# Optimization experiments

Measured on AMD Instinct MI355X. Metric: run time of the kernel, lower is better.

Reference implementation:

```python
import jax, jax.numpy as jnp
import numpy as np

N, E, DIN, DH, DE, DOUT, G = 100000, 1600000, 64, 128, 16, 1, 256

def setup_inputs() -> dict:
    key = jax.random.key(0)
    ks = jax.random.split(key, 16)
    p = lambda k, s: (jax.random.normal(k, s, dtype=jnp.float32) * 0.05)
    return {
        "x": jax.random.normal(ks[0], (N, DIN), dtype=jnp.float32),
        "edge_index": jax.random.randint(ks[1], (2, E), 0, N, dtype=jnp.int64),
        "edge_attr": jax.random.normal(ks[2], (E, DE), dtype=jnp.float32),
        "batch": jnp.sort(jax.random.randint(ks[3], (N,), 0, G, dtype=jnp.int64)),
        # GINEConv 1: edge lin (edge_dim -> input_dim) + mlp1 (DIN->DH->DH)
        "ew1": p(ks[4], (DIN, DE)), "eb1": p(ks[5], (DIN,)),
        "w1a": p(ks[6], (DH, DIN)), "b1a": p(ks[7], (DH,)),
        "w1b": p(ks[8], (DH, DH)), "b1b": p(ks[9], (DH,)),
        # GINEConv 2: edge lin (edge_dim -> hidden_dim) + mlp2 (DH->DH->DH)
        "ew2": p(ks[10], (DH, DE)), "eb2": p(ks[11], (DH,)),
        "w2a": p(ks[12], (DH, DH)), "b2a": p(ks[13], (DH,)),
        "w2b": p(ks[14], (DH, DH)), "b2b": p(ks[15], (DH,)),
        "wf": p(jax.random.fold_in(key, 99), (DOUT, DH)),
        "bf": jnp.zeros((DOUT,), dtype=jnp.float32),
    }

def _gine(x, src, dst, edge_attr, ew, eb, wa, ba, wb, bb):
    # message = relu(x[src] + Lin(edge_attr)); sum-aggregate at dst; eps=0
    msg = jax.nn.relu(x[src] + edge_attr @ ew.T + eb)          # [E, D]
    aggr = jax.ops.segment_sum(msg, dst, num_segments=x.shape[0])
    h = x + aggr                                               # (1+eps)*x + aggr, eps=0
    h = jax.nn.relu(h @ wa.T + ba)
    return h @ wb.T + bb

def reference(x, edge_index, edge_attr, batch, ew1, eb1, w1a, b1a, w1b, b1b,
              ew2, eb2, w2a, b2a, w2b, b2b, wf, bf):
    src, dst = edge_index[0], edge_index[1]
    h = _gine(x, src, dst, edge_attr, ew1, eb1, w1a, b1a, w1b, b1b)
    h = jax.nn.relu(h)  # dropout is identity in eval mode
    h = _gine(h, src, dst, edge_attr, ew2, eb2, w2a, b2a, w2b, b2b)
    h = jax.nn.relu(h)
    # global mean pool over graphs
    sums = jax.ops.segment_sum(h, batch, num_segments=G)       # [G, DH]
    cnts = jax.ops.segment_sum(jnp.ones((h.shape[0],), h.dtype), batch, num_segments=G)
    pooled = sums / jnp.maximum(cnts, 1.0)[:, None]
    return pooled @ wf.T + bf                                  # [G, DOUT]
```

## Files before the change

kernel.cpp:

```cpp
#include <hip/hip_runtime.h>

#define DINc 64
#define DHc  128
#define DEc  16
#define Gc   256
#define Rrep 64
#define SCB  1024

typedef unsigned short u16;
typedef unsigned int   u32;
typedef __attribute__((ext_vector_type(8))) short bf8;
typedef __attribute__((ext_vector_type(4))) short bf4;
typedef __attribute__((ext_vector_type(4))) float f4;
typedef __attribute__((ext_vector_type(4))) unsigned int u32x4;
typedef _Float16 h2t __attribute__((ext_vector_type(2)));

__device__ __forceinline__ u16 f2b(float f) {
  u32 u = __builtin_bit_cast(u32, f);
  u32 r = u + 0x7FFFu + ((u >> 16) & 1u);
  return (u16)(r >> 16);
}
__device__ __forceinline__ float b2f(u16 h) {
  u32 u = ((u32)h) << 16;
  return __builtin_bit_cast(float, u);
}
__device__ __forceinline__ float blo(u32 v) { return __builtin_bit_cast(float, v << 16); }
__device__ __forceinline__ float bhi(u32 v) { return __builtin_bit_cast(float, v & 0xFFFF0000u); }
__device__ __forceinline__ u32 pkbf(float a, float b) {
  return ((u32)f2b(b) << 16) | (u32)f2b(a);
}
__device__ __forceinline__ u32 pkh(float a, float b) {
  u16 ua = __builtin_bit_cast(u16, (_Float16)a);
  u16 ub = __builtin_bit_cast(u16, (_Float16)b);
  return ((u32)ub << 16) | ua;
}
__device__ __forceinline__ float fd2(u32 a, u32 b, float c) {
  return __builtin_amdgcn_fdot2(__builtin_bit_cast(h2t, a),
                                __builtin_bit_cast(h2t, b), c, false);
}

__global__ __launch_bounds__(256) void k_prep(
    const float* __restrict__ w1a, const float* __restrict__ w1b,
    const float* __restrict__ w2a, const float* __restrict__ w2b,
    u16* __restrict__ wts,
    const int* __restrict__ dstA, const int nE, int* __restrict__ deg) {
  const int b = blockIdx.x;
  if (b < 28) {
    const int i = b * 256 + threadIdx.x;
    const float* src; int off;
    if      (i < 1024) { src = w1a; off = i; }
    else if (i < 3072) { src = w1b; off = i - 1024; }
    else if (i < 5120) { src = w2a; off = i - 3072; }
    else if (i < 7168) { src = w2b; off = i - 5120; }
    else return;
    float4 f0 = *(const float4*)(src + (size_t)off * 8);
    float4 f1 = *(const float4*)(src + (size_t)off * 8 + 4);
    bf8 v;
    v[0]=(short)f2b(f0.x); v[1]=(short)f2b(f0.y); v[2]=(short)f2b(f0.z); v[3]=(short)f2b(f0.w);
    v[4]=(short)f2b(f1.x); v[5]=(short)f2b(f1.y); v[6]=(short)f2b(f1.z); v[7]=(short)f2b(f1.w);
    *(bf8*)(wts + (size_t)i * 8) = v;
  } else {
    const int nb = gridDim.x - 28;
    for (int i = (b - 28) * 256 + threadIdx.x; i < nE; i += nb * 256)
      atomicAdd(&deg[dstA[i]], 1);
  }
}

__global__ __launch_bounds__(256) void k_scan_blk(const int* __restrict__ deg,
                                                  int* __restrict__ bsum, const int nN) {
  const int b = blockIdx.x, t = threadIdx.x;
  const int i0 = b * SCB + t * 4;
  int s = 0;
  #pragma unroll
  for (int q = 0; q < 4; ++q) { const int i = i0 + q; if (i < nN) s += deg[i]; }
  #pragma unroll
  for (int off = 32; off > 0; off >>= 1) s += __shfl_down(s, off);
  __shared__ int ws[4];
  if ((t & 63) == 0) ws[t >> 6] = s;
  __syncthreads();
  if (t == 0) bsum[b] = ws[0] + ws[1] + ws[2] + ws[3];
}

__global__ __launch_bounds__(256) void k_scan_fin(const int* __restrict__ deg,
                                                  const int* __restrict__ bsum,
                                                  int* __restrict__ rowptr,
                                                  const int nN, const int nB) {
  const int b = blockIdx.x, t = threadIdx.x;
  int p = 0;
  for (int i = t; i < b; i += 256) p += bsum[i];
  #pragma unroll
  for (int off = 32; off > 0; off >>= 1) p += __shfl_down(p, off);
  __shared__ int ws[4];
  __shared__ int sc[256];
  if ((t & 63) == 0) ws[t >> 6] = p;
  const int i0 = b * SCB + t * 4;
  int vals[4]; int s = 0;
  #pragma unroll
  for (int q = 0; q < 4; ++q) { const int i = i0 + q; vals[q] = (i < nN) ? deg[i] : 0; s += vals[q]; }
  sc[t] = s;
  __syncthreads();
  const int boff = ws[0] + ws[1] + ws[2] + ws[3];
  for (int off = 1; off < 256; off <<= 1) {
    int u = (t >= off) ? sc[t - off] : 0;
    __syncthreads();
    sc[t] += u;
    __syncthreads();
  }
  int run = boff + sc[t] - s;
  #pragma unroll
  for (int q = 0; q < 4; ++q) { const int i = i0 + q; if (i < nN) rowptr[i] = run; run += vals[q]; }
  if (b == nB - 1 && t == 255) rowptr[nN] = run;
}

__global__ __launch_bounds__(256) void k_fill(const int* __restrict__ dstA,
                                              const int* __restrict__ srcA,
                                              const float* __restrict__ ea, const int nE,
                                              const int* __restrict__ rowptr,
                                              int* __restrict__ cursor,
                                              int* __restrict__ srcC,
                                              int* __restrict__ dstC,
                                              u16* __restrict__ ea16) {
  for (int i = blockIdx.x * 256 + threadIdx.x; i < nE; i += gridDim.x * 256) {
    const int d = dstA[i];
    const int pos = rowptr[d] + atomicAdd(&cursor[d], 1);
    srcC[pos] = srcA[i];
    dstC[pos] = d;
    const float4* ep = (const float4*)(ea + (size_t)i * 16);
    float4 a0 = ep[0], a1 = ep[1], a2 = ep[2], a3 = ep[3];
    u32x4 w0, w1;
    w0[0] = pkh(a0.x, a0.y); w0[1] = pkh(a0.z, a0.w);
    w0[2] = pkh(a1.x, a1.y); w0[3] = pkh(a1.z, a1.w);
    w1[0] = pkh(a2.x, a2.y); w1[1] = pkh(a2.z, a2.w);
    w1[2] = pkh(a3.x, a3.y); w1[3] = pkh(a3.z, a3.w);
    *(u32x4*)(ea16 + (size_t)pos * 16)     = w0;
    *(u32x4*)(ea16 + (size_t)pos * 16 + 8) = w1;
  }
}

__device__ __forceinline__ int span_lb(const int* __restrict__ rp, int nN, int target) {
  int lo = 0, hi = nN;
  while (lo < hi) { int m = (lo + hi) >> 1; if (rp[m] < target) lo = m + 1; else hi = m; }
  return lo;
}

#define STORE_N(NODE) do { \
  if (PL == 2) *(u32*)(agg + (size_t)(NODE) * 128 + lane * 2) = pkbf(acc0, acc1); \
  else         agg[(size_t)(NODE) * 64 + lane] = f2b(acc0); \
} while (0)
#define STORE_Z(NODE) do { \
  if (PL == 2) *(u32*)(agg + (size_t)(NODE) * 128 + lane * 2) = 0u; \
  else         agg[(size_t)(NODE) * 64 + lane] = 0; \
} while (0)
#define BCHK(EIDX) do { \
  if ((bmask >> (EIDX)) & 1ull) { \
    const int nd = __builtin_amdgcn_readlane(dl, (EIDX)); \
    if (cur >= n0) STORE_N(cur); \
    for (int m = cur + 1; m < nd; ++m) STORE_Z(m); \
    acc0 = 0.f; acc1 = 0.f; cur = nd; \
  } \
} while (0)
#define ACC_EDGE(EIDX, Q) do { \
  u32x4 r0 = *(const u32x4*)&E[(EIDX)][0]; \
  u32x4 r1 = *(const u32x4*)&E[(EIDX)][4]; \
  if (PL == 1) { \
    float v = ebr[0]; \
    v = fd2(r0[0], wpk[0], v); v = fd2(r0[1], wpk[1], v); \
    v = fd2(r0[2], wpk[2], v); v = fd2(r0[3], wpk[3], v); \
    v = fd2(r1[0], wpk[4], v); v = fd2(r1[1], wpk[5], v); \
    v = fd2(r1[2], wpk[6], v); v = fd2(r1[3], wpk[7], v); \
    const float xval = XF ? xs[Q] : blo(xv[Q]); \
    acc0 += fmaxf(xval + v, 0.f); \
  } else { \
    float v0 = ebr[0], v1 = ebr[1]; \
    v0 = fd2(r0[0], wpk[0], v0); v1 = fd2(r0[0], wpk[8],  v1); \
    v0 = fd2(r0[1], wpk[1], v0); v1 = fd2(r0[1], wpk[9],  v1); \
    v0 = fd2(r0[2], wpk[2], v0); v1 = fd2(r0[2], wpk[10], v1); \
    v0 = fd2(r0[3], wpk[3], v0); v1 = fd2(r0[3], wpk[11], v1); \
    v0 = fd2(r1[0], wpk[4], v0); v1 = fd2(r1[0], wpk[12], v1); \
    v0 = fd2(r1[1], wpk[5], v0); v1 = fd2(r1[1], wpk[13], v1); \
    v0 = fd2(r1[2], wpk[6], v0); v1 = fd2(r1[2], wpk[14], v1); \
    v0 = fd2(r1[3], wpk[7], v0); v1 = fd2(r1[3], wpk[15], v1); \
    acc0 += fmaxf(blo(xv[Q]) + v0, 0.f); \
    acc1 += fmaxf(bhi(xv[Q]) + v1, 0.f); \
  } \
} while (0)

template<int D, bool XF>
__global__ __launch_bounds__(256) void gather4(
    const float* __restrict__ xf, const u16* __restrict__ xb,
    const int* __restrict__ srcC, const int* __restrict__ dstC,
    const u16* __restrict__ ea16,
    const float* __restrict__ ewg, const float* __restrict__ ebg,
    const int* __restrict__ rowptr, u16* __restrict__ agg,
    const int nN, const int nE)
{
  constexpr int PL = D / 64;
  __shared__ u32 eas[4][64][8];
  const int lane = threadIdx.x & 63, wv = threadIdx.x >> 6;
  u32 (*E)[8] = eas[wv];

  u32 wpk[8 * PL]; float ebr[PL];
  #pragma unroll
  for (int p = 0; p < PL; ++p) {
    const int d = lane * PL + p;
    ebr[p] = ebg[d];
    #pragma unroll
    for (int j = 0; j < 8; ++j)
      wpk[p * 8 + j] = pkh(ewg[d * 16 + 2 * j], ewg[d * 16 + 2 * j + 1]);
  }

  const int wgid = blockIdx.x * 4 + wv;
  const int nw   = gridDim.x * 4;
  const int t0 = (int)((long long)nE * wgid / nw);
  const int t1 = (int)((long long)nE * (wgid + 1) / nw);
  const int n0 = span_lb(rowptr, nN, t0);
  const int n1 = (wgid == nw - 1) ? nN : span_lb(rowptr, nN, t1);
  if (n0 >= n1) return;
  const int e0 = rowptr[n0], e1 = rowptr[n1];

  float acc0 = 0.f, acc1 = 0.f;
  int cur = n0 - 1;

  for (int chunk = e0; chunk < e1; chunk += 64) {
    const int cnt = min(64, e1 - chunk);
    int sid = (lane < cnt) ? srcC[chunk + lane] : 0;
    int dl  = (lane < cnt) ? dstC[chunk + lane] : -1;
    const int pd = __shfl_up(dl, 1);
    const bool bnd = (lane < cnt) && (dl != ((lane == 0) ? cur : pd));
    const unsigned long long bmask = __ballot(bnd);

    if (lane < cnt) {
      u32x4 a = *(const u32x4*)(ea16 + (size_t)(chunk + lane) * 16);
      u32x4 b = *(const u32x4*)(ea16 + (size_t)(chunk + lane) * 16 + 8);
      *(u32x4*)&E[lane][0] = a;
      *(u32x4*)&E[lane][4] = b;
    }

    if (cnt == 64) {
      #pragma unroll 1
      for (int i = 0; i < 64; i += 8) {
        u32 xv[8]; float xs[8];
        #pragma unroll
        for (int q = 0; q < 8; ++q) {
          const int s = __builtin_amdgcn_readlane(sid, i + q);
          if (XF) xs[q] = xf[(size_t)s * D + lane];
          else    xv[q] = *(const u32*)(xb + (size_t)s * D + lane * 2);
        }
        const u32 gm = (u32)(bmask >> i) & 0xFFu;
        if (gm == 0) {
          #pragma unroll
          for (int q = 0; q < 8; ++q) ACC_EDGE(i + q, q);
        } else {
          #pragma unroll
          for (int q = 0; q < 8; ++q) { BCHK(i + q); ACC_EDGE(i + q, q); }
        }
      }
    } else {
      for (int i = 0; i < cnt; i += 8) {
        const int g = min(8, cnt - i);
        u32 xv[8]; float xs[8];
        #pragma unroll
        for (int q = 0; q < 8; ++q) {
          if (q < g) {
            const int s = __builtin_amdgcn_readlane(sid, i + q);
            if (XF) xs[q] = xf[(size_t)s * D + lane];
            else    xv[q] = *(const u32*)(xb + (size_t)s * D + lane * 2);
          }
        }
        #pragma unroll
        for (int q = 0; q < 8; ++q) {
          if (q < g) { BCHK(i + q); ACC_EDGE(i + q, q); }
        }
      }
    }
  }
  if (cur >= n0) STORE_N(cur);
  for (int m = cur + 1; m < n1; ++m) STORE_Z(m);
}

template<int IN, bool XF>
__global__ __launch_bounds__(256) void k_l1(
    const float* __restrict__ xf, const u16* __restrict__ xbm,
    const u16* __restrict__ agb,
    const u16* __restrict__ waB, const float* __restrict__ ba,
    u16* __restrict__ tout, const int nN)
{
  __shared__ u16 wa_s[DHc * IN];
  __shared__ float ba_s[DHc];
  const int tid = threadIdx.x;
  constexpr int INC = IN / 8;
  for (int c = tid; c < DHc * INC; c += 256) {
    const int row = c / INC, kc = (c % INC) * 8;
    bf8 v = *(const bf8*)(waB + (size_t)row * IN + kc);
    *(bf8*)(wa_s + ((row * IN + kc) ^ ((row & 7) << 3))) = v;
  }
  if (tid < DHc) ba_s[tid] = ba[tid];
  __syncthreads();
  const int lane = tid & 63, wv = tid >> 6;
  const int lr = lane & 15, l4 = lane >> 4;
  const int nT = (nN + 15) >> 4;
  for (int tile = blockIdx.x * 4 + wv; tile < nT; tile += gridDim.x * 4) {
    const int node = tile * 16 + lr;
    const int n = min(node, nN - 1);
    bf8 bfr[IN / 32];
    #pragma unroll
    for (int ks = 0; ks < IN / 32; ++ks) {
      const int k0 = ks * 32 + l4 * 8;
      bf8 av = *(const bf8*)(agb + (size_t)n * IN + k0);
      bf8 v;
      if (XF) {
        float4 x0 = *(const float4*)(xf + (size_t)n * IN + k0);
        float4 x1 = *(const float4*)(xf + (size_t)n * IN + k0 + 4);
        v[0] = (short)f2b(x0.x + b2f((u16)av[0]));
        v[1] = (short)f2b(x0.y + b2f((u16)av[1]));
        v[2] = (short)f2b(x0.z + b2f((u16)av[2]));
        v[3] = (short)f2b(x0.w + b2f((u16)av[3]));
        v[4] = (short)f2b(x1.x + b2f((u16)av[4]));
        v[5] = (short)f2b(x1.y + b2f((u16)av[5]));
        v[6] = (short)f2b(x1.z + b2f((u16)av[6]));
        v[7] = (short)f2b(x1.w + b2f((u16)av[7]));
      } else {
        bf8 xv = *(const bf8*)(xbm + (size_t)n * IN + k0);
        #pragma unroll
        for (int j = 0; j < 8; ++j)
          v[j] = (short)f2b(b2f((u16)xv[j]) + b2f((u16)av[j]));
      }
      bfr[ks] = v;
    }
    const bool valid = node < nN;
    #pragma unroll
    for (int jt = 0; jt < 8; ++jt) {
      f4 c = {0.f, 0.f, 0.f, 0.f};
      #pragma unroll
      for (int ks = 0; ks < IN / 32; ++ks) {
        bf8 a = *(const bf8*)(wa_s + (((jt * 16 + lr) * IN + ks * 32 + l4 * 8) ^ ((lr & 7) << 3)));
        c = __builtin_amdgcn_mfma_f32_16x16x32_bf16(a, bfr[ks], c, 0, 0, 0);
      }
      if (valid) {
        float4 bav = *(const float4*)(ba_s + jt * 16 + l4 * 4);
        bf4 tv;
        tv[0] = (short)f2b(fmaxf(c[0] + bav.x, 0.f));
        tv[1] = (short)f2b(fmaxf(c[1] + bav.y, 0.f));
        tv[2] = (short)f2b(fmaxf(c[2] + bav.z, 0.f));
        tv[3] = (short)f2b(fmaxf(c[3] + bav.w, 0.f));
        *(bf4*)(tout + (size_t)node * DHc + jt * 16 + l4 * 4) = tv;
      }
    }
  }
}

template<bool FINAL>
__global__ __launch_bounds__(256) void k_l2(
    const u16* __restrict__ tin, const u16* __restrict__ wbB,
    const float* __restrict__ bb, u16* __restrict__ hout,
    const int* __restrict__ batch, float* __restrict__ sums, const int nN)
{
  __shared__ u16 wb_s[DHc * DHc];
  __shared__ float bb_s[DHc];
  const int tid = threadIdx.x;
  for (int c = tid; c < DHc * 16; c += 256) {
    const int row = c >> 4, kc = (c & 15) * 8;
    bf8 v = *(const bf8*)(wbB + (size_t)row * DHc + kc);
    *(bf8*)(wb_s + ((row * DHc + kc) ^ ((row & 7) << 3))) = v;
  }
  if (tid < DHc) bb_s[tid] = bb[tid];
  __syncthreads();
  const int lane = tid & 63, wv = tid >> 6;
  const int lr = lane & 15, l4 = lane >> 4;
  const int nT = (nN + 15) >> 4;
  const int gw0 = blockIdx.x * 4 + wv;
  const int rep = gw0 & (Rrep - 1);
  for (int tile = gw0; tile < nT; tile += gridDim.x * 4) {
    const int node0 = tile * 16;
    const int node = node0 + lr;
    const int n = min(node, nN - 1);
    bf8 tb[4];
    #pragma unroll
    for (int ks = 0; ks < 4; ++ks)
      tb[ks] = *(const bf8*)(tin + (size_t)n * DHc + ks * 32 + l4 * 8);
    const bool valid = node < nN;
    int gl = 0, g0 = 0; bool uni = false;
    if (FINAL) {
      gl = batch[n];
      g0 = __shfl(gl, 0);
      uni = __all(gl == g0) && (node0 + 16 <= nN);
    }
    #pragma unroll
    for (int jt = 0; jt < 8; ++jt) {
      f4 c = {0.f, 0.f, 0.f, 0.f};
      #pragma unroll
      for (int ks = 0; ks < 4; ++ks) {
        bf8 a = *(const bf8*)(wb_s + (((jt * 16 + lr) * DHc + ks * 32 + l4 * 8) ^ ((lr & 7) << 3)));
        c = __builtin_amdgcn_mfma_f32_16x16x32_bf16(a, tb[ks], c, 0, 0, 0);
      }
      float4 bbv = *(const float4*)(bb_s + jt * 16 + l4 * 4);
      float o0 = fmaxf(c[0] + bbv.x, 0.f);
      float o1 = fmaxf(c[1] + bbv.y, 0.f);
      float o2 = fmaxf(c[2] + bbv.z, 0.f);
      float o3 = fmaxf(c[3] + bbv.w, 0.f);
      if (!FINAL) {
        if (valid) {
          bf4 hv;
          hv[0] = (short)f2b(o0); hv[1] = (short)f2b(o1);
          hv[2] = (short)f2b(o2); hv[3] = (short)f2b(o3);
          *(bf4*)(hout + (size_t)node * DHc + jt * 16 + l4 * 4) = hv;
        }
      } else {
        if (uni) {
          #pragma unroll
          for (int off = 1; off < 16; off <<= 1) {
            o0 += __shfl_xor(o0, off);
            o1 += __shfl_xor(o1, off);
            o2 += __shfl_xor(o2, off);
            o3 += __shfl_xor(o3, off);
          }
          if (lr == 0) {
            float* dp = sums + ((size_t)rep * Gc + g0) * DHc + jt * 16 + l4 * 4;
            atomicAdd(dp + 0, o0); atomicAdd(dp + 1, o1);
            atomicAdd(dp + 2, o2); atomicAdd(dp + 3, o3);
          }
        } else if (valid) {
          float* dp = sums + ((size_t)rep * Gc + gl) * DHc + jt * 16 + l4 * 4;
          atomicAdd(dp + 0, o0); atomicAdd(dp + 1, o1);
          atomicAdd(dp + 2, o2); atomicAdd(dp + 3, o3);
        }
      }
    }
  }
}

__global__ __launch_bounds__(128) void pool_final(
    const float* __restrict__ sums, const int* __restrict__ batch,
    const float* __restrict__ wf, const float* __restrict__ bf,
    float* __restrict__ out, const int nN)
{
  const int g = blockIdx.x;
  const int j = threadIdx.x;
  float s = 0.f;
  for (int r = 0; r < Rrep; ++r) s += sums[((size_t)r * Gc + g) * DHc + j];
  int lo = 0, hi = nN;
  while (lo < hi) { int m = (lo + hi) >> 1; if (batch[m] < g) lo = m + 1; else hi = m; }
  int lo2 = lo, hi2 = nN;
  while (lo2 < hi2) { int m = (lo2 + hi2) >> 1; if (batch[m] < g + 1) lo2 = m + 1; else hi2 = m; }
  const float ct = fmaxf((float)(lo2 - lo), 1.f);
  __shared__ float red[128];
  red[j] = (s / ct) * wf[j];
  __syncthreads();
  for (int off = 64; off > 0; off >>= 1) { if (j < off) red[j] += red[j + off]; __syncthreads(); }
  if (j == 0) out[g] = red[0] + bf[0];
}

extern "C" void kernel_launch(void* const* d_in, const int* in_sizes, int n_in,
                              void* d_out, int out_size, void* d_ws, size_t ws_size,
                              hipStream_t stream) {
  const float* x    = (const float*)d_in[0];
  const int*   ei   = (const int*)d_in[1];
  const float* ea   = (const float*)d_in[2];
  const int*   batch= (const int*)d_in[3];
  const float* ew1  = (const float*)d_in[4];
  const float* eb1  = (const float*)d_in[5];
  const float* w1a  = (const float*)d_in[6];
  const float* b1a  = (const float*)d_in[7];
  const float* w1b  = (const float*)d_in[8];
  const float* b1b  = (const float*)d_in[9];
  const float* ew2  = (const float*)d_in[10];
  const float* eb2  = (const float*)d_in[11];
  const float* w2a  = (const float*)d_in[12];
  const float* b2a  = (const float*)d_in[13];
  const float* w2b  = (const float*)d_in[14];
  const float* b2b  = (const float*)d_in[15];
  const float* wf   = (const float*)d_in[16];
  const float* bf   = (const float*)d_in[17];
  float* out = (float*)d_out;

  const int nN = in_sizes[0] / DINc;
  const int nE = in_sizes[1] / 2;
  const int* srcA = ei;
  const int* dstA = ei + nE;

  char* wsb = (char*)d_ws;
  size_t o = 0;
  u16*   h1b    = (u16*)  (wsb + o); o += (size_t)nN * DHc * 2;
  u16*   tbuf   = (u16*)  (wsb + o); o += (size_t)nN * DHc * 2;
  u16*   agb    = (u16*)  (wsb + o); o += (size_t)nN * DHc * 2;
  float* sums   = (float*)(wsb + o); o += (size_t)Rrep * Gc * DHc * 4;
  int*   deg    = (int*)  (wsb + o); o += (size_t)nN * 4;
  int*   cursor = (int*)  (wsb + o); o += (size_t)nN * 4;
  int*   rowptr = (int*)  (wsb + o); o += (size_t)(nN + 1) * 4;
  int*   bsum   = (int*)  (wsb + o); o += (size_t)((nN + SCB - 1) / SCB) * 4; o = (o + 15) & ~(size_t)15;
  int*   srcC   = (int*)  (wsb + o); o += (size_t)nE * 4;
  int*   dstC   = (int*)  (wsb + o); o += (size_t)nE * 4; o = (o + 15) & ~(size_t)15;
  u16*   ea16   = (u16*)  (wsb + o); o += (size_t)nE * 16 * 2;
  u16*   wts    = (u16*)  (wsb + o); o += (size_t)57344 * 2;
  u16* w1ab = wts;
  u16* w1bb = wts + 8192;
  u16* w2ab = wts + 8192 + 16384;
  u16* w2bb = wts + 8192 + 32768;
  (void)ws_size; (void)n_in; (void)out_size;

  hipMemsetAsync(sums, 0, (size_t)Rrep * Gc * DHc * 4, stream);
  hipMemsetAsync(deg, 0, (size_t)nN * 8, stream);

  const int nB = (nN + SCB - 1) / SCB;
  k_prep<<<28 + 512, 256, 0, stream>>>(w1a, w1b, w2a, w2b, wts, dstA, nE, deg);
  k_scan_blk<<<nB, 256, 0, stream>>>(deg, bsum, nN);
  k_scan_fin<<<nB, 256, 0, stream>>>(deg, bsum, rowptr, nN, nB);
  k_fill<<<1024, 256, 0, stream>>>(dstA, srcA, ea, nE, rowptr, cursor, srcC, dstC, ea16);

  const int nT = (nN + 15) / 16;
  const int mg = (nT + 3) / 4;
  gather4<DINc, true><<<2048, 256, 0, stream>>>(x, nullptr, srcC, dstC, ea16,
                                                ew1, eb1, rowptr, agb, nN, nE);
  k_l1<DINc, true><<<mg, 256, 0, stream>>>(x, nullptr, agb, w1ab, b1a, tbuf, nN);
  k_l2<false><<<mg, 256, 0, stream>>>(tbuf, w1bb, b1b, h1b, nullptr, nullptr, nN);
  gather4<DHc, false><<<2048, 256, 0, stream>>>(nullptr, h1b, srcC, dstC, ea16,
                                                ew2, eb2, rowptr, agb, nN, nE);
  k_l1<DHc, false><<<mg, 256, 0, stream>>>(nullptr, h1b, agb, w2ab, b2a, tbuf, nN);
  k_l2<true><<<mg, 256, 0, stream>>>(tbuf, w2bb, b2b, nullptr, batch, sums, nN);
  pool_final<<<Gc, 128, 0, stream>>>(sums, batch, wf, bf, out, nN);
}
```

Baseline: 574.8 us.

## Replace CSR-permuted edge copies with edge-index indirection and overlap fp16 conversion

```diff
diff --git a/kernel.cpp b/kernel.cpp
--- a/kernel.cpp
+++ b/kernel.cpp
@@ -43,7 +43,8 @@
     const float* __restrict__ w1a, const float* __restrict__ w1b,
     const float* __restrict__ w2a, const float* __restrict__ w2b,
     u16* __restrict__ wts,
-    const int* __restrict__ dstA, const int nE, int* __restrict__ deg) {
+    const int* __restrict__ dstA, const int nE, int* __restrict__ deg,
+    const float* __restrict__ ea, u16* __restrict__ ea16e) {
   const int b = blockIdx.x;
   if (b < 28) {
     const int i = b * 256 + threadIdx.x;
@@ -59,10 +60,20 @@
     v[0]=(short)f2b(f0.x); v[1]=(short)f2b(f0.y); v[2]=(short)f2b(f0.z); v[3]=(short)f2b(f0.w);
     v[4]=(short)f2b(f1.x); v[5]=(short)f2b(f1.y); v[6]=(short)f2b(f1.z); v[7]=(short)f2b(f1.w);
     *(bf8*)(wts + (size_t)i * 8) = v;
+  } else if (b < 540) {
+    for (int i = (b - 28) * 256 + threadIdx.x; i < nE; i += 512 * 256)
+      atomicAdd(&deg[dstA[i]], 1);
   } else {
-    const int nb = gridDim.x - 28;
-    for (int i = (b - 28) * 256 + threadIdx.x; i < nE; i += nb * 256)
-      atomicAdd(&deg[dstA[i]], 1);
+    const int nb = gridDim.x - 540;
+    const int n8 = nE * 2;
+    for (int i = (b - 540) * 256 + threadIdx.x; i < n8; i += nb * 256) {
+      float4 f0 = *(const float4*)(ea + (size_t)i * 8);
+      float4 f1 = *(const float4*)(ea + (size_t)i * 8 + 4);
+      u32x4 w;
+      w[0] = pkh(f0.x, f0.y); w[1] = pkh(f0.z, f0.w);
+      w[2] = pkh(f1.x, f1.y); w[3] = pkh(f1.z, f1.w);
+      *(u32x4*)(ea16e + (size_t)i * 8) = w;
+    }
   }
 }
 
@@ -112,28 +123,14 @@
   if (b == nB - 1 && t == 255) rowptr[nN] = run;
 }
 
-__global__ __launch_bounds__(256) void k_fill(const int* __restrict__ dstA,
-                                              const int* __restrict__ srcA,
-                                              const float* __restrict__ ea, const int nE,
+__global__ __launch_bounds__(256) void k_fill(const int* __restrict__ dstA, const int nE,
                                               const int* __restrict__ rowptr,
                                               int* __restrict__ cursor,
-                                              int* __restrict__ srcC,
-                                              int* __restrict__ dstC,
-                                              u16* __restrict__ ea16) {
+                                              int* __restrict__ eidxC) {
   for (int i = blockIdx.x * 256 + threadIdx.x; i < nE; i += gridDim.x * 256) {
     const int d = dstA[i];
     const int pos = rowptr[d] + atomicAdd(&cursor[d], 1);
-    srcC[pos] = srcA[i];
-    dstC[pos] = d;
-    const float4* ep = (const float4*)(ea + (size_t)i * 16);
-    float4 a0 = ep[0], a1 = ep[1], a2 = ep[2], a3 = ep[3];
-    u32x4 w0, w1;
-    w0[0] = pkh(a0.x, a0.y); w0[1] = pkh(a0.z, a0.w);
-    w0[2] = pkh(a1.x, a1.y); w0[3] = pkh(a1.z, a1.w);
-    w1[0] = pkh(a2.x, a2.y); w1[1] = pkh(a2.z, a2.w);
-    w1[2] = pkh(a3.x, a3.y); w1[3] = pkh(a3.z, a3.w);
-    *(u32x4*)(ea16 + (size_t)pos * 16)     = w0;
-    *(u32x4*)(ea16 + (size_t)pos * 16 + 8) = w1;
+    eidxC[pos] = i;
   }
 }
 
@@ -186,10 +183,11 @@
 } while (0)
 
 template<int D, bool XF>
-__global__ __launch_bounds__(256) void gather4(
+__global__ __launch_bounds__(256) void gather5(
     const float* __restrict__ xf, const u16* __restrict__ xb,
-    const int* __restrict__ srcC, const int* __restrict__ dstC,
-    const u16* __restrict__ ea16,
+    const int* __restrict__ eidxC,
+    const int* __restrict__ srcA, const int* __restrict__ dstA,
+    const u16* __restrict__ ea16e,
     const float* __restrict__ ewg, const float* __restrict__ ebg,
     const int* __restrict__ rowptr, u16* __restrict__ agg,
     const int nN, const int nE)
@@ -223,15 +221,16 @@
 
   for (int chunk = e0; chunk < e1; chunk += 64) {
     const int cnt = min(64, e1 - chunk);
-    int sid = (lane < cnt) ? srcC[chunk + lane] : 0;
-    int dl  = (lane < cnt) ? dstC[chunk + lane] : -1;
+    const int eid = (lane < cnt) ? eidxC[chunk + lane] : 0;
+    int sid = (lane < cnt) ? srcA[eid] : 0;
+    int dl  = (lane < cnt) ? dstA[eid] : -1;
     const int pd = __shfl_up(dl, 1);
     const bool bnd = (lane < cnt) && (dl != ((lane == 0) ? cur : pd));
     const unsigned long long bmask = __ballot(bnd);
 
     if (lane < cnt) {
-      u32x4 a = *(const u32x4*)(ea16 + (size_t)(chunk + lane) * 16);
-      u32x4 b = *(const u32x4*)(ea16 + (size_t)(chunk + lane) * 16 + 8);
+      u32x4 a = *(const u32x4*)(ea16e + (size_t)eid * 16);
+      u32x4 b = *(const u32x4*)(ea16e + (size_t)eid * 16 + 8);
       *(u32x4*)&E[lane][0] = a;
       *(u32x4*)&E[lane][4] = b;
     }
@@ -488,9 +487,8 @@
   int*   cursor = (int*)  (wsb + o); o += (size_t)nN * 4;
   int*   rowptr = (int*)  (wsb + o); o += (size_t)(nN + 1) * 4;
   int*   bsum   = (int*)  (wsb + o); o += (size_t)((nN + SCB - 1) / SCB) * 4; o = (o + 15) & ~(size_t)15;
-  int*   srcC   = (int*)  (wsb + o); o += (size_t)nE * 4;
-  int*   dstC   = (int*)  (wsb + o); o += (size_t)nE * 4; o = (o + 15) & ~(size_t)15;
-  u16*   ea16   = (u16*)  (wsb + o); o += (size_t)nE * 16 * 2;
+  int*   eidxC  = (int*)  (wsb + o); o += (size_t)nE * 4; o = (o + 15) & ~(size_t)15;
+  u16*   ea16e  = (u16*)  (wsb + o); o += (size_t)nE * 16 * 2;
   u16*   wts    = (u16*)  (wsb + o); o += (size_t)57344 * 2;
   u16* w1ab = wts;
   u16* w1bb = wts + 8192;
@@ -502,18 +500,19 @@
   hipMemsetAsync(deg, 0, (size_t)nN * 8, stream);
 
   const int nB = (nN + SCB - 1) / SCB;
-  k_prep<<<28 + 512, 256, 0, stream>>>(w1a, w1b, w2a, w2b, wts, dstA, nE, deg);
+  k_prep<<<28 + 512 + 256, 256, 0, stream>>>(w1a, w1b, w2a, w2b, wts,
+                                             dstA, nE, deg, ea, ea16e);
   k_scan_blk<<<nB, 256, 0, stream>>>(deg, bsum, nN);
   k_scan_fin<<<nB, 256, 0, stream>>>(deg, bsum, rowptr, nN, nB);
-  k_fill<<<1024, 256, 0, stream>>>(dstA, srcA, ea, nE, rowptr, cursor, srcC, dstC, ea16);
+  k_fill<<<1024, 256, 0, stream>>>(dstA, nE, rowptr, cursor, eidxC);
 
   const int nT = (nN + 15) / 16;
   const int mg = (nT + 3) / 4;
-  gather4<DINc, true><<<2048, 256, 0, stream>>>(x, nullptr, srcC, dstC, ea16,
+  gather5<DINc, true><<<2048, 256, 0, stream>>>(x, nullptr, eidxC, srcA, dstA, ea16e,
                                                 ew1, eb1, rowptr, agb, nN, nE);
   k_l1<DINc, true><<<mg, 256, 0, stream>>>(x, nullptr, agb, w1ab, b1a, tbuf, nN);
   k_l2<false><<<mg, 256, 0, stream>>>(tbuf, w1bb, b1b, h1b, nullptr, nullptr, nN);
-  gather4<DHc, false><<<2048, 256, 0, stream>>>(nullptr, h1b, srcC, dstC, ea16,
+  gather5<DHc, false><<<2048, 256, 0, stream>>>(nullptr, h1b, eidxC, srcA, dstA, ea16e,
                                                 ew2, eb2, rowptr, agb, nN, nE);
   k_l1<DHc, false><<<mg, 256, 0, stream>>>(nullptr, h1b, agb, w2ab, b2a, tbuf, nN);
   k_l2<true><<<mg, 256, 0, stream>>>(tbuf, w2bb, b2b, nullptr, batch, sums, nN);
```

After: 677.3 us. 17.8% more time.
